# Kernel optimization log

Measured on AMD Instinct MI355X. Metric: run time of the kernel, lower is better.

## Reference

```python
import jax, jax.numpy as jnp
import numpy as np

N_NODES = 100000
N_EDGES = 1200000
N_GRAPHS = 256
IN_C, HID_C, OUT_C = 5, 64, 2


def gcn_conv(x, src, dst, W, b, n_nodes):
    """PyG GCNConv: h = x@W; add self-loops; deg from target col (edge weight 1);
    norm = deg^{-1/2}[src]*deg^{-1/2}[dst]; scatter-add messages into dst; + bias."""
    loop = jnp.arange(n_nodes, dtype=src.dtype)
    s = jnp.concatenate([src, loop])
    d = jnp.concatenate([dst, loop])
    deg = jax.ops.segment_sum(jnp.ones_like(d, dtype=x.dtype), d, num_segments=n_nodes)
    dinv = jnp.where(deg > 0, jax.lax.rsqrt(deg), 0.0)
    norm = dinv[s] * dinv[d]                     # [E+N]
    h = x @ W                                    # [N, out]
    msg = h[s] * norm[:, None]                   # gather + scale  [E+N, out]
    out = jax.ops.segment_sum(msg, d, num_segments=n_nodes)  # scatter-add
    return out + b


def setup_inputs() -> dict:
    key = jax.random.key(0)
    ks = jax.random.split(key, 10)
    x = jax.random.normal(ks[0], (N_NODES, IN_C), dtype=jnp.float32)
    edge_index = jax.random.randint(ks[1], (2, N_EDGES), 0, N_NODES, dtype=jnp.int64)
    batch = jnp.sort(jax.random.randint(ks[2], (N_NODES,), 0, N_GRAPHS, dtype=jnp.int64))
    def glorot(k, fan_in, fan_out):
        lim = np.sqrt(6.0 / (fan_in + fan_out))
        return jax.random.uniform(k, (fan_in, fan_out), jnp.float32, -lim, lim)
    W1 = glorot(ks[3], IN_C, HID_C)
    b1 = jnp.zeros((HID_C,), jnp.float32)
    W2 = glorot(ks[4], HID_C, HID_C)
    b2 = jnp.zeros((HID_C,), jnp.float32)
    Wfc = glorot(ks[5], HID_C, OUT_C)
    bfc = jnp.zeros((OUT_C,), jnp.float32)
    return {"x": x, "edge_index": edge_index, "batch": batch,
            "W1": W1, "b1": b1, "W2": W2, "b2": b2, "Wfc": Wfc, "bfc": bfc}


def reference(x, edge_index, batch, W1, b1, W2, b2, Wfc, bfc):
    src, dst = edge_index[0], edge_index[1]
    h = jax.nn.relu(gcn_conv(x, src, dst, W1, b1, N_NODES))
    h = jax.nn.relu(gcn_conv(h, src, dst, W2, b2, N_NODES))
    # global_mean_pool over graph ids in `batch`
    sums = jax.ops.segment_sum(h, batch, num_segments=N_GRAPHS)          # [G, H]
    cnts = jax.ops.segment_sum(jnp.ones((h.shape[0],), h.dtype), batch,
                               num_segments=N_GRAPHS)                    # [G]
    pooled = sums / jnp.maximum(cnts, 1.0)[:, None]
    return pooled @ Wfc + bfc                                            # [G, 2]
```

## Files before the change

### kernel.cpp

```cpp
#include <hip/hip_runtime.h>

#define N_NODES 100000
#define N_EDGES 1200000
#define N_GRAPHS 256
#define IN_C 5
#define HID_C 64
#define OUT_C 2

#define BSH 7
#define BNODES 128
#define NB ((N_NODES + BNODES - 1) / BNODES)
#define CAPB 2048
#define EPB 2048
#define NBLK_E ((N_EDGES + EPB - 1) / EPB)
#define GNPW 8
#define L1NPW 8

typedef unsigned int uint32;

__device__ __forceinline__ uint32 f2bf(float f) {
    uint32 x = __float_as_uint(f);
    return (x + 0x7FFFu + ((x >> 16) & 1u)) >> 16;
}
__device__ __forceinline__ float bflo(uint32 r) { return __uint_as_float(r << 16); }
__device__ __forceinline__ float bfhi(uint32 r) { return __uint_as_float(r & 0xFFFF0000u); }

__global__ void k_bscatter(const int* __restrict__ src, const int* __restrict__ dst,
                           int* __restrict__ bcnt, int* __restrict__ pairs,
                           float* __restrict__ pooled) {
    __shared__ int h[NB];
    if (blockIdx.x < (N_GRAPHS * HID_C) / 256)
        pooled[blockIdx.x * 256 + threadIdx.x] = 0.f;
    for (int i = threadIdx.x; i < NB; i += blockDim.x) h[i] = 0;
    __syncthreads();
    int e0 = blockIdx.x * EPB;
    int e1 = e0 + EPB; if (e1 > N_EDGES) e1 = N_EDGES;
    for (int e = e0 + threadIdx.x; e < e1; e += blockDim.x)
        atomicAdd(&h[dst[e] >> BSH], 1);
    __syncthreads();
    for (int i = threadIdx.x; i < NB; i += blockDim.x)
        if (h[i]) h[i] = (i << 11) + atomicAdd(&bcnt[i], h[i]);
    __syncthreads();
    for (int e = e0 + threadIdx.x; e < e1; e += blockDim.x) {
        int d = dst[e];
        int pos = atomicAdd(&h[d >> BSH], 1);
        pairs[pos] = ((d & (BNODES - 1)) << 17) | src[e];
    }
}

__global__ void k_bsort_xs(const int* __restrict__ pairs, const int* __restrict__ bcnt,
                           const float* __restrict__ x,
                           int* __restrict__ csr, int* __restrict__ rs,
                           int* __restrict__ cnt, float* __restrict__ dinv,
                           float* __restrict__ xs) {
    __shared__ int hist[BNODES];
    __shared__ int tmp[BNODES];
    __shared__ int cur[BNODES];
    __shared__ float sdv[BNODES];
    int b = blockIdx.x;
    int t = threadIdx.x;
    int base = b << BSH;
    if (t < BNODES) hist[t] = 0;
    __syncthreads();
    int s = b << 11;
    int n = bcnt[b];
    for (int i = t; i < n; i += 256)
        atomicAdd(&hist[pairs[s + i] >> 17], 1);
    __syncthreads();
    int v = (t < BNODES) ? hist[t] : 0;
    if (t < BNODES) tmp[t] = v;
    __syncthreads();
    for (int off = 1; off < BNODES; off <<= 1) {
        int a = (t < BNODES && t >= off) ? tmp[t - off] : 0;
        __syncthreads();
        if (t < BNODES) tmp[t] += a;
        __syncthreads();
    }
    float dv_t = rsqrtf((float)v + 1.0f);
    if (t < BNODES) {
        cur[t] = tmp[t] - v;
        sdv[t] = dv_t;
        if (base + t < N_NODES) {
            rs[base + t] = s + tmp[t] - v;
            cnt[base + t] = v;
            dinv[base + t] = dv_t;
        }
    }
    __syncthreads();
    for (int i = t; i < n; i += 256) {
        int p = pairs[s + i];
        int pos = atomicAdd(&cur[p >> 17], 1);
        csr[s + pos] = p & 0x1FFFF;
    }
    for (int i = t; i < BNODES * 8; i += 256) {
        int nl = i >> 3, k = i & 7;
        int node = base + nl;
        if (node < N_NODES && k < IN_C)
            xs[(unsigned)node * 8 + k] = x[(unsigned)node * IN_C + k] * sdv[nl];
    }
}

__global__ void __launch_bounds__(256) k_l1(
        const float* __restrict__ xs, const int* __restrict__ csr,
        const int* __restrict__ rs, const int* __restrict__ cnt,
        const float* __restrict__ dinv, const float* __restrict__ b1,
        const float* __restrict__ W1, const float* __restrict__ W2,
        uint32* __restrict__ g2t) {
    __shared__ __align__(16) float sagg[4][L1NPW][8];
    __shared__ __align__(16) float srow[4][2][HID_C];
    int tid = threadIdx.x;
    int w = tid >> 6;
    int lane = tid & 63;
    int base = (blockIdx.x * 4 + w) * L1NPW;

    int g = lane >> 3, l = lane & 7;
    int v = base + g;
    float a0 = 0.f, a1 = 0.f, a2 = 0.f, a3 = 0.f, a4 = 0.f;
    if (v < N_NODES) {
        int k0 = rs[v];
        int n = cnt[v];
        if (l == 0) {
            float4 p = *(const float4*)&xs[(unsigned)v * 8];
            a0 = p.x; a1 = p.y; a2 = p.z; a3 = p.w;
            a4 = xs[(unsigned)v * 8 + 4];
        }
        int i = l;
        int un = (i < n) ? csr[k0 + i] : -1;
        while (un >= 0) {
            int u = un;
            i += 8;
            un = (i < n) ? csr[k0 + i] : -1;
            float4 p = *(const float4*)&xs[(unsigned)u * 8];
            float p4 = xs[(unsigned)u * 8 + 4];
            a0 += p.x; a1 += p.y; a2 += p.z; a3 += p.w; a4 += p4;
        }
    }
#pragma unroll
    for (int off = 4; off; off >>= 1) {
        a0 += __shfl_xor(a0, off);
        a1 += __shfl_xor(a1, off);
        a2 += __shfl_xor(a2, off);
        a3 += __shfl_xor(a3, off);
        a4 += __shfl_xor(a4, off);
    }
    if (l == 0 && v < N_NODES) {
        *(float4*)&sagg[w][g][0] = make_float4(a0, a1, a2, a3);
        sagg[w][g][4] = a4;
    }

    int half = lane >> 5, c2 = lane & 31;
    int kb = half << 5;
    float2 w1r[IN_C];
#pragma unroll
    for (int k = 0; k < IN_C; ++k)
        w1r[k] = *(const float2*)&W1[k * HID_C + 2 * c2];
    float2 w2r[32];
#pragma unroll
    for (int j = 0; j < 32; ++j)
        w2r[j] = *(const float2*)&W2[(kb + j) * HID_C + 2 * c2];
    float2 bias = *(const float2*)&b1[2 * c2];

    for (int gg = 0; gg < L1NPW; ++gg) {
        int node = base + gg;
        if (node >= N_NODES) break;
        float dv = dinv[node];
        float4 qa = *(const float4*)&sagg[w][gg][0];
        float q4 = sagg[w][gg][4];
        float s0 = qa.x * w1r[0].x + qa.y * w1r[1].x + qa.z * w1r[2].x
                 + qa.w * w1r[3].x + q4 * w1r[4].x;
        float s1 = qa.x * w1r[0].y + qa.y * w1r[1].y + qa.z * w1r[2].y
                 + qa.w * w1r[3].y + q4 * w1r[4].y;
        float h0 = fmaxf(s0 * dv + bias.x, 0.f);
        float h1 = fmaxf(s1 * dv + bias.y, 0.f);
        int buf = gg & 1;
        if (half == 0) *(float2*)&srow[w][buf][2 * c2] = make_float2(h0, h1);
        float t0 = 0.f, t1 = 0.f;
#pragma unroll
        for (int jj = 0; jj < 8; ++jj) {
            float4 hv = *(const float4*)&srow[w][buf][kb + 4 * jj];
            t0 += hv.x * w2r[4 * jj + 0].x + hv.y * w2r[4 * jj + 1].x
                + hv.z * w2r[4 * jj + 2].x + hv.w * w2r[4 * jj + 3].x;
            t1 += hv.x * w2r[4 * jj + 0].y + hv.y * w2r[4 * jj + 1].y
                + hv.z * w2r[4 * jj + 2].y + hv.w * w2r[4 * jj + 3].y;
        }
        t0 += __shfl_xor(t0, 32);
        t1 += __shfl_xor(t1, 32);
        if (half == 0)
            g2t[(unsigned)node * 32 + c2] = (f2bf(t1 * dv) << 16) | f2bf(t0 * dv);
    }
}

__global__ void __launch_bounds__(256) k_gather2p(
        const uint32* __restrict__ g, const int* __restrict__ csr,
        const int* __restrict__ rs, const int* __restrict__ cnt,
        const float* __restrict__ dinv, const float* __restrict__ b,
        const int* __restrict__ batch, float* __restrict__ pooled) {
    int wv = __builtin_amdgcn_readfirstlane(
        blockIdx.x * (blockDim.x >> 6) + (threadIdx.x >> 6));
    int n0 = wv * GNPW;
    if (n0 >= N_NODES) return;
    int n1 = n0 + GNPW; if (n1 > N_NODES) n1 = N_NODES;
    int lane = threadIdx.x & 63;
    int half = lane >> 5;
    int c2 = lane & 31;
    float bias0 = b[2 * c2], bias1 = b[2 * c2 + 1];
    float p0 = 0.f, p1 = 0.f;
    int curg = -1;
    for (int vb = n0; vb < n1; vb += 2) {
        int v = vb + half;
        int valid = (v < n1);
        int k0 = 0, n = 0;
        float s0 = 0.f, s1 = 0.f;
        if (valid) {
            k0 = rs[v];
            n = cnt[v];
            uint32 r = g[(unsigned)v * 32 + c2];
            s0 = bflo(r); s1 = bfhi(r);
        }
        int i = 0;
        for (; i + 7 < n; i += 8) {
            int u0 = csr[k0 + i + 0], u1 = csr[k0 + i + 1];
            int u2 = csr[k0 + i + 2], u3 = csr[k0 + i + 3];
            int u4 = csr[k0 + i + 4], u5 = csr[k0 + i + 5];
            int u6 = csr[k0 + i + 6], u7 = csr[k0 + i + 7];
            uint32 r0 = g[(unsigned)u0 * 32 + c2];
            uint32 r1 = g[(unsigned)u1 * 32 + c2];
            uint32 r2 = g[(unsigned)u2 * 32 + c2];
            uint32 r3 = g[(unsigned)u3 * 32 + c2];
            uint32 r4 = g[(unsigned)u4 * 32 + c2];
            uint32 r5 = g[(unsigned)u5 * 32 + c2];
            uint32 r6 = g[(unsigned)u6 * 32 + c2];
            uint32 r7 = g[(unsigned)u7 * 32 + c2];
            s0 += ((bflo(r0) + bflo(r1)) + (bflo(r2) + bflo(r3)))
                + ((bflo(r4) + bflo(r5)) + (bflo(r6) + bflo(r7)));
            s1 += ((bfhi(r0) + bfhi(r1)) + (bfhi(r2) + bfhi(r3)))
                + ((bfhi(r4) + bfhi(r5)) + (bfhi(r6) + bfhi(r7)));
        }
        for (; i + 3 < n; i += 4) {
            int u0 = csr[k0 + i + 0], u1 = csr[k0 + i + 1];
            int u2 = csr[k0 + i + 2], u3 = csr[k0 + i + 3];
            uint32 r0 = g[(unsigned)u0 * 32 + c2];
            uint32 r1 = g[(unsigned)u1 * 32 + c2];
            uint32 r2 = g[(unsigned)u2 * 32 + c2];
            uint32 r3 = g[(unsigned)u3 * 32 + c2];
            s0 += (bflo(r0) + bflo(r1)) + (bflo(r2) + bflo(r3));
            s1 += (bfhi(r0) + bfhi(r1)) + (bfhi(r2) + bfhi(r3));
        }
        for (; i < n; ++i) {
            uint32 r = g[(unsigned)csr[k0 + i] * 32 + c2];
            s0 += bflo(r); s1 += bfhi(r);
        }
        if (valid) {
            float dv = dinv[v];
            float o0 = fmaxf(s0 * dv + bias0, 0.f);
            float o1 = fmaxf(s1 * dv + bias1, 0.f);
            int gg = batch[v];
            if (gg != curg) {
                if (curg >= 0) {
                    atomicAdd(&pooled[curg * HID_C + 2 * c2], p0);
                    atomicAdd(&pooled[curg * HID_C + 2 * c2 + 1], p1);
                }
                p0 = 0.f; p1 = 0.f; curg = gg;
            }
            p0 += o0; p1 += o1;
        }
    }
    if (curg >= 0) {
        atomicAdd(&pooled[curg * HID_C + 2 * c2], p0);
        atomicAdd(&pooled[curg * HID_C + 2 * c2 + 1], p1);
    }
}

__global__ void k_fc(const float* __restrict__ pooled, const int* __restrict__ batch,
                     const float* __restrict__ Wfc, const float* __restrict__ bfc,
                     float* __restrict__ out) {
    int g = blockIdx.x;
    int c = threadIdx.x;
    int lo = 0, hi = N_NODES;
    while (lo < hi) { int mid = (lo + hi) >> 1; if (batch[mid] < g) lo = mid + 1; else hi = mid; }
    int start = lo;
    hi = N_NODES;
    while (lo < hi) { int mid = (lo + hi) >> 1; if (batch[mid] < g + 1) lo = mid + 1; else hi = mid; }
    int n = lo - start;
    float pv = pooled[g * HID_C + c] / (float)(n > 0 ? n : 1);
    float o0 = pv * Wfc[c * OUT_C + 0];
    float o1 = pv * Wfc[c * OUT_C + 1];
#pragma unroll
    for (int off = 32; off > 0; off >>= 1) {
        o0 += __shfl_down(o0, off);
        o1 += __shfl_down(o1, off);
    }
    if (c == 0) {
        out[g * OUT_C + 0] = o0 + bfc[0];
        out[g * OUT_C + 1] = o1 + bfc[1];
    }
}

extern "C" void kernel_launch(void* const* d_in, const int* in_sizes, int n_in,
                              void* d_out, int out_size, void* d_ws, size_t ws_size,
                              hipStream_t stream) {
    const float* x    = (const float*)d_in[0];
    const int*   ei   = (const int*)d_in[1];
    const int*   src  = ei;
    const int*   dst  = ei + N_EDGES;
    const int*   batch= (const int*)d_in[2];
    const float* W1   = (const float*)d_in[3];
    const float* b1   = (const float*)d_in[4];
    const float* W2   = (const float*)d_in[5];
    const float* b2   = (const float*)d_in[6];
    const float* Wfc  = (const float*)d_in[7];
    const float* bfc  = (const float*)d_in[8];
    float* out = (float*)d_out;

    float*  ws     = (float*)d_ws;
    int*    bcnt   = (int*)ws;
    float*  pooled = ws + 1024;
    float*  dinv   = pooled + 16384;
    int*    cnt    = (int*)(dinv + 100352);
    int*    rs     = cnt + 100352;
    int*    pairs  = rs + 100352;
    int*    csr    = pairs + (NB * CAPB);
    float*  xs     = (float*)(csr + (NB * CAPB));
    uint32* g2tab  = (uint32*)(xs + N_NODES * 8);

    hipMemsetAsync(bcnt, 0, 1024 * sizeof(int), stream);

    k_bscatter<<<NBLK_E, 256, 0, stream>>>(src, dst, bcnt, pairs, pooled);
    k_bsort_xs<<<NB, 256, 0, stream>>>(pairs, bcnt, x, csr, rs, cnt, dinv, xs);

    {
        int blocks = (N_NODES + 4 * L1NPW - 1) / (4 * L1NPW);
        k_l1<<<blocks, 256, 0, stream>>>(xs, csr, rs, cnt, dinv, b1, W1, W2, g2tab);
    }

    {
        int waves = (N_NODES + GNPW - 1) / GNPW;
        int blocks = (waves + 3) / 4;
        k_gather2p<<<blocks, 256, 0, stream>>>(g2tab, csr, rs, cnt, dinv, b2, batch, pooled);
    }

    k_fc<<<N_GRAPHS, 64, 0, stream>>>(pooled, batch, Wfc, bfc, out);
}
```

Baseline: 209.3 us.

## Restructure layer-2 gather: 16 lanes per node, 8 nodes per wave concurrently

The layer-2 gather kernel now assigns 16 lanes per node, each loading a uint2 (4 bf16 channels), so a wave handles 4 nodes at once and interleaves two node sets, giving more independent loads in flight. The pooled sum is reduced across the wave with shuffles and committed with a single set of atomics when all 8 nodes share a graph, otherwise per-node atomics. Launch bounds add a min-blocks hint. N_NODES must be a multiple of 8 with no tail guard, which holds for 100000, and loop divergence between the paired nodes may waste lanes.

```diff
diff --git a/kernel.cpp b/kernel.cpp
--- a/kernel.cpp
+++ b/kernel.cpp
@@ -190,7 +190,10 @@
     }
 }
 
-__global__ void __launch_bounds__(256) k_gather2p(
+#define LDU2(d, u) uint2 d = *(const uint2*)&g[(unsigned)(u) * 32 + 2 * c4]
+#define ACC4(s0, s1, s2, s3, r) { s0 += bflo(r.x); s1 += bfhi(r.x); \
+                                  s2 += bflo(r.y); s3 += bfhi(r.y); }
+__global__ void __launch_bounds__(256, 4) k_gather2p(
         const uint32* __restrict__ g, const int* __restrict__ csr,
         const int* __restrict__ rs, const int* __restrict__ cnt,
         const float* __restrict__ dinv, const float* __restrict__ b,
@@ -199,75 +202,131 @@
         blockIdx.x * (blockDim.x >> 6) + (threadIdx.x >> 6));
     int n0 = wv * GNPW;
     if (n0 >= N_NODES) return;
-    int n1 = n0 + GNPW; if (n1 > N_NODES) n1 = N_NODES;
     int lane = threadIdx.x & 63;
-    int half = lane >> 5;
-    int c2 = lane & 31;
-    float bias0 = b[2 * c2], bias1 = b[2 * c2 + 1];
-    float p0 = 0.f, p1 = 0.f;
-    int curg = -1;
-    for (int vb = n0; vb < n1; vb += 2) {
-        int v = vb + half;
-        int valid = (v < n1);
-        int k0 = 0, n = 0;
-        float s0 = 0.f, s1 = 0.f;
-        if (valid) {
-            k0 = rs[v];
-            n = cnt[v];
-            uint32 r = g[(unsigned)v * 32 + c2];
-            s0 = bflo(r); s1 = bfhi(r);
+    int sub = lane >> 4;
+    int c4 = lane & 15;
+    int va = n0 + sub, vb = n0 + 4 + sub;
+    int ka = rs[va], na = cnt[va];
+    int kb = rs[vb], nb = cnt[vb];
+    float dva = dinv[va], dvb = dinv[vb];
+    int ga = batch[va], gb = batch[vb];
+    float4 bias = *(const float4*)&b[4 * c4];
+    LDU2(rsa, va); LDU2(rsb, vb);
+    float a0 = bflo(rsa.x), a1 = bfhi(rsa.x), a2 = bflo(rsa.y), a3 = bfhi(rsa.y);
+    float y0 = bflo(rsb.x), y1 = bfhi(rsb.x), y2 = bflo(rsb.y), y3 = bfhi(rsb.y);
+    int ia = 0, ib = 0;
+    while (ia + 7 < na && ib + 7 < nb) {
+        int u0 = csr[ka+ia+0], u1 = csr[ka+ia+1], u2 = csr[ka+ia+2], u3 = csr[ka+ia+3];
+        int u4 = csr[ka+ia+4], u5 = csr[ka+ia+5], u6 = csr[ka+ia+6], u7 = csr[ka+ia+7];
+        int w0 = csr[kb+ib+0], w1 = csr[kb+ib+1], w2 = csr[kb+ib+2], w3 = csr[kb+ib+3];
+        int w4 = csr[kb+ib+4], w5 = csr[kb+ib+5], w6 = csr[kb+ib+6], w7 = csr[kb+ib+7];
+        LDU2(p0, u0); LDU2(p1, u1); LDU2(p2, u2); LDU2(p3, u3);
+        LDU2(p4, u4); LDU2(p5, u5); LDU2(p6, u6); LDU2(p7, u7);
+        LDU2(q0, w0); LDU2(q1, w1); LDU2(q2, w2); LDU2(q3, w3);
+        LDU2(q4, w4); LDU2(q5, w5); LDU2(q6, w6); LDU2(q7, w7);
+        ACC4(a0, a1, a2, a3, p0); ACC4(a0, a1, a2, a3, p1);
+        ACC4(a0, a1, a2, a3, p2); ACC4(a0, a1, a2, a3, p3);
+        ACC4(a0, a1, a2, a3, p4); ACC4(a0, a1, a2, a3, p5);
+        ACC4(a0, a1, a2, a3, p6); ACC4(a0, a1, a2, a3, p7);
+        ACC4(y0, y1, y2, y3, q0); ACC4(y0, y1, y2, y3, q1);
+        ACC4(y0, y1, y2, y3, q2); ACC4(y0, y1, y2, y3, q3);
+        ACC4(y0, y1, y2, y3, q4); ACC4(y0, y1, y2, y3, q5);
+        ACC4(y0, y1, y2, y3, q6); ACC4(y0, y1, y2, y3, q7);
+        ia += 8; ib += 8;
+    }
+    while (ia + 7 < na) {
+        int u0 = csr[ka+ia+0], u1 = csr[ka+ia+1], u2 = csr[ka+ia+2], u3 = csr[ka+ia+3];
+        int u4 = csr[ka+ia+4], u5 = csr[ka+ia+5], u6 = csr[ka+ia+6], u7 = csr[ka+ia+7];
+        LDU2(p0, u0); LDU2(p1, u1); LDU2(p2, u2); LDU2(p3, u3);
+        LDU2(p4, u4); LDU2(p5, u5); LDU2(p6, u6); LDU2(p7, u7);
+        ACC4(a0, a1, a2, a3, p0); ACC4(a0, a1, a2, a3, p1);
+        ACC4(a0, a1, a2, a3, p2); ACC4(a0, a1, a2, a3, p3);
+        ACC4(a0, a1, a2, a3, p4); ACC4(a0, a1, a2, a3, p5);
+        ACC4(a0, a1, a2, a3, p6); ACC4(a0, a1, a2, a3, p7);
+        ia += 8;
+    }
+    while (ib + 7 < nb) {
+        int w0 = csr[kb+ib+0], w1 = csr[kb+ib+1], w2 = csr[kb+ib+2], w3 = csr[kb+ib+3];
+        int w4 = csr[kb+ib+4], w5 = csr[kb+ib+5], w6 = csr[kb+ib+6], w7 = csr[kb+ib+7];
+        LDU2(q0, w0); LDU2(q1, w1); LDU2(q2, w2); LDU2(q3, w3);
+        LDU2(q4, w4); LDU2(q5, w5); LDU2(q6, w6); LDU2(q7, w7);
+        ACC4(y0, y1, y2, y3, q0); ACC4(y0, y1, y2, y3, q1);
+        ACC4(y0, y1, y2, y3, q2); ACC4(y0, y1, y2, y3, q3);
+        ACC4(y0, y1, y2, y3, q4); ACC4(y0, y1, y2, y3, q5);
+        ACC4(y0, y1, y2, y3, q6); ACC4(y0, y1, y2, y3, q7);
+        ib += 8;
+    }
+    while (ia + 3 < na && ib + 3 < nb) {
+        int u0 = csr[ka+ia+0], u1 = csr[ka+ia+1], u2 = csr[ka+ia+2], u3 = csr[ka+ia+3];
+        int w0 = csr[kb+ib+0], w1 = csr[kb+ib+1], w2 = csr[kb+ib+2], w3 = csr[kb+ib+3];
+        LDU2(p0, u0); LDU2(p1, u1); LDU2(p2, u2); LDU2(p3, u3);
+        LDU2(q0, w0); LDU2(q1, w1); LDU2(q2, w2); LDU2(q3, w3);
+        ACC4(a0, a1, a2, a3, p0); ACC4(a0, a1, a2, a3, p1);
+        ACC4(a0, a1, a2, a3, p2); ACC4(a0, a1, a2, a3, p3);
+        ACC4(y0, y1, y2, y3, q0); ACC4(y0, y1, y2, y3, q1);
+        ACC4(y0, y1, y2, y3, q2); ACC4(y0, y1, y2, y3, q3);
+        ia += 4; ib += 4;
+    }
+    while (ia + 3 < na) {
+        int u0 = csr[ka+ia+0], u1 = csr[ka+ia+1], u2 = csr[ka+ia+2], u3 = csr[ka+ia+3];
+        LDU2(p0, u0); LDU2(p1, u1); LDU2(p2, u2); LDU2(p3, u3);
+        ACC4(a0, a1, a2, a3, p0); ACC4(a0, a1, a2, a3, p1);
+        ACC4(a0, a1, a2, a3, p2); ACC4(a0, a1, a2, a3, p3);
+        ia += 4;
+    }
+    while (ib + 3 < nb) {
+        int w0 = csr[kb+ib+0], w1 = csr[kb+ib+1], w2 = csr[kb+ib+2], w3 = csr[kb+ib+3];
+        LDU2(q0, w0); LDU2(q1, w1); LDU2(q2, w2); LDU2(q3, w3);
+        ACC4(y0, y1, y2, y3, q0); ACC4(y0, y1, y2, y3, q1);
+        ACC4(y0, y1, y2, y3, q2); ACC4(y0, y1, y2, y3, q3);
+        ib += 4;
+    }
+    while (ia < na && ib < nb) {
+        int u0 = csr[ka + ia], w0 = csr[kb + ib];
+        LDU2(p0, u0); LDU2(q0, w0);
+        ACC4(a0, a1, a2, a3, p0); ACC4(y0, y1, y2, y3, q0);
+        ++ia; ++ib;
+    }
+    while (ia < na) {
+        LDU2(p0, csr[ka + ia]);
+        ACC4(a0, a1, a2, a3, p0);
+        ++ia;
+    }
+    while (ib < nb) {
+        LDU2(q0, csr[kb + ib]);
+        ACC4(y0, y1, y2, y3, q0);
+        ++ib;
+    }
+    float oa0 = fmaxf(a0 * dva + bias.x, 0.f);
+    float oa1 = fmaxf(a1 * dva + bias.y, 0.f);
+    float oa2 = fmaxf(a2 * dva + bias.z, 0.f);
+    float oa3 = fmaxf(a3 * dva + bias.w, 0.f);
+    float ob0 = fmaxf(y0 * dvb + bias.x, 0.f);
+    float ob1 = fmaxf(y1 * dvb + bias.y, 0.f);
+    float ob2 = fmaxf(y2 * dvb + bias.z, 0.f);
+    float ob3 = fmaxf(y3 * dvb + bias.w, 0.f);
+    int g0 = __builtin_amdgcn_readfirstlane(ga);
+    if (__all(ga == g0) && __all(gb == g0)) {
+        float f0 = oa0 + ob0, f1 = oa1 + ob1, f2 = oa2 + ob2, f3 = oa3 + ob3;
+        f0 += __shfl_xor(f0, 16); f0 += __shfl_xor(f0, 32);
+        f1 += __shfl_xor(f1, 16); f1 += __shfl_xor(f1, 32);
+        f2 += __shfl_xor(f2, 16); f2 += __shfl_xor(f2, 32);
+        f3 += __shfl_xor(f3, 16); f3 += __shfl_xor(f3, 32);
+        if (sub == 0) {
+            atomicAdd(&pooled[g0 * HID_C + 4 * c4 + 0], f0);
+            atomicAdd(&pooled[g0 * HID_C + 4 * c4 + 1], f1);
+            atomicAdd(&pooled[g0 * HID_C + 4 * c4 + 2], f2);
+            atomicAdd(&pooled[g0 * HID_C + 4 * c4 + 3], f3);
         }
-        int i = 0;
-        for (; i + 7 < n; i += 8) {
-            int u0 = csr[k0 + i + 0], u1 = csr[k0 + i + 1];
-            int u2 = csr[k0 + i + 2], u3 = csr[k0 + i + 3];
-            int u4 = csr[k0 + i + 4], u5 = csr[k0 + i + 5];
-            int u6 = csr[k0 + i + 6], u7 = csr[k0 + i + 7];
-            uint32 r0 = g[(unsigned)u0 * 32 + c2];
-            uint32 r1 = g[(unsigned)u1 * 32 + c2];
-            uint32 r2 = g[(unsigned)u2 * 32 + c2];
-            uint32 r3 = g[(unsigned)u3 * 32 + c2];
-            uint32 r4 = g[(unsigned)u4 * 32 + c2];
-            uint32 r5 = g[(unsigned)u5 * 32 + c2];
-            uint32 r6 = g[(unsigned)u6 * 32 + c2];
-            uint32 r7 = g[(unsigned)u7 * 32 + c2];
-            s0 += ((bflo(r0) + bflo(r1)) + (bflo(r2) + bflo(r3)))
-                + ((bflo(r4) + bflo(r5)) + (bflo(r6) + bflo(r7)));
-            s1 += ((bfhi(r0) + bfhi(r1)) + (bfhi(r2) + bfhi(r3)))
-                + ((bfhi(r4) + bfhi(r5)) + (bfhi(r6) + bfhi(r7)));
-        }
-        for (; i + 3 < n; i += 4) {
-            int u0 = csr[k0 + i + 0], u1 = csr[k0 + i + 1];
-            int u2 = csr[k0 + i + 2], u3 = csr[k0 + i + 3];
-            uint32 r0 = g[(unsigned)u0 * 32 + c2];
-            uint32 r1 = g[(unsigned)u1 * 32 + c2];
-            uint32 r2 = g[(unsigned)u2 * 32 + c2];
-            uint32 r3 = g[(unsigned)u3 * 32 + c2];
-            s0 += (bflo(r0) + bflo(r1)) + (bflo(r2) + bflo(r3));
-            s1 += (bfhi(r0) + bfhi(r1)) + (bfhi(r2) + bfhi(r3));
-        }
-        for (; i < n; ++i) {
-            uint32 r = g[(unsigned)csr[k0 + i] * 32 + c2];
-            s0 += bflo(r); s1 += bfhi(r);
-        }
-        if (valid) {
-            float dv = dinv[v];
-            float o0 = fmaxf(s0 * dv + bias0, 0.f);
-            float o1 = fmaxf(s1 * dv + bias1, 0.f);
-            int gg = batch[v];
-            if (gg != curg) {
-                if (curg >= 0) {
-                    atomicAdd(&pooled[curg * HID_C + 2 * c2], p0);
-                    atomicAdd(&pooled[curg * HID_C + 2 * c2 + 1], p1);
-                }
-                p0 = 0.f; p1 = 0.f; curg = gg;
-            }
-            p0 += o0; p1 += o1;
-        }
-    }
-    if (curg >= 0) {
-        atomicAdd(&pooled[curg * HID_C + 2 * c2], p0);
-        atomicAdd(&pooled[curg * HID_C + 2 * c2 + 1], p1);
+    } else {
+        atomicAdd(&pooled[ga * HID_C + 4 * c4 + 0], oa0);
+        atomicAdd(&pooled[ga * HID_C + 4 * c4 + 1], oa1);
+        atomicAdd(&pooled[ga * HID_C + 4 * c4 + 2], oa2);
+        atomicAdd(&pooled[ga * HID_C + 4 * c4 + 3], oa3);
+        atomicAdd(&pooled[gb * HID_C + 4 * c4 + 0], ob0);
+        atomicAdd(&pooled[gb * HID_C + 4 * c4 + 1], ob1);
+        atomicAdd(&pooled[gb * HID_C + 4 * c4 + 2], ob2);
+        atomicAdd(&pooled[gb * HID_C + 4 * c4 + 3], ob3);
     }
 }
 
```

Measured after the change: 205.0 us (median of 2 runs). -2.0%, faster.
